# Optimization experiments

Measured on AMD Instinct MI355X. Metric: run time of the kernel, lower is better.

## Reference

```python
import jax, jax.numpy as jnp
import numpy as np

N_NODES = 100000
N_EDGES = 1600000
D_IN, D_HID, D_OUT = 128, 16, 32


def setup_inputs() -> dict:
    key = jax.random.key(0)
    k1, k2, k3, k4, k5 = jax.random.split(key, 5)
    features = jax.random.normal(k1, (N_NODES, D_IN), dtype=jnp.float32)
    src = jax.random.randint(k2, (N_EDGES,), 0, N_NODES, dtype=jnp.int32)
    dst = jax.random.randint(k3, (N_EDGES,), 0, N_NODES, dtype=jnp.int32)
    # linear layer params (PyTorch Linear: y = x @ W.T + b); store as (in, out)
    s1 = 1.0 / np.sqrt(D_IN)
    s2 = 1.0 / np.sqrt(D_HID)
    W1 = jax.random.uniform(k4, (D_IN, D_HID), minval=-s1, maxval=s1, dtype=jnp.float32)
    b1 = jnp.zeros((D_HID,), dtype=jnp.float32)
    W2 = jax.random.uniform(k5, (D_HID, D_OUT), minval=-s2, maxval=s2, dtype=jnp.float32)
    b2 = jnp.zeros((D_OUT,), dtype=jnp.float32)
    return {"features": features, "src": src, "dst": dst,
            "W1": W1, "b1": b1, "W2": W2, "b2": b2}


def _gcn_layer(h, src, dst, W, b):
    # copy_src + sum: aggregate neighbor (src) features onto dst nodes
    agg = jax.ops.segment_sum(h[src], dst, num_segments=N_NODES)
    return agg @ W + b


def reference(features, src, dst, W1, b1, W2, b2):
    x = jax.nn.relu(_gcn_layer(features, src, dst, W1, b1))
    x = _gcn_layer(x, src, dst, W2, b2)
    return x
```

## Files before the change

### kernel.cpp

```cpp
#include <hip/hip_runtime.h>
#include <hip/hip_bf16.h>

#define N_NODES 100000
#define N_EDGES 1600000
#define D_IN    128
#define D_HID   16
#define D_OUT   32

#define BSHIFT 8
#define BNODES 256
#define NB 391
#define NBPAD 512
#define SCHUNK 4096
#define SBLOCKS 391
#define MMBLOCKS 1563
#define SLAB 4608
#define NOSTRIDE 257

#define SS_HIST   0
#define SS_LBASE  2048
#define SS_GBASE  4096
#define SS_TSCAN  5696
#define SS_SORTED 6720
#define SS_BID    23104
#define SS_BYTES  31296

__device__ inline float bf_lo(unsigned dw) { return __uint_as_float(dw << 16); }
__device__ inline float bf_hi(unsigned dw) { return __uint_as_float(dw & 0xffff0000u); }
__device__ inline unsigned bf_pack(float f0, float f1) {
    union { __hip_bfloat16 h[2]; unsigned u; } pu;
    pu.h[0] = __float2bfloat16(f0);
    pu.h[1] = __float2bfloat16(f1);
    return pu.u;
}
__device__ inline void acc4(float* a, uint2 w) {
    a[0] += bf_lo(w.x); a[1] += bf_hi(w.x);
    a[2] += bf_lo(w.y); a[3] += bf_hi(w.y);
}

__global__ __launch_bounds__(256) void k_fused1(const float* __restrict__ feat,
                                                const float* __restrict__ W1,
                                                const int* __restrict__ src,
                                                const int* __restrict__ dst,
                                                int* __restrict__ cursor,
                                                unsigned* __restrict__ pairs,
                                                unsigned* __restrict__ Yu) {
    __shared__ __align__(16) char smem[SS_BYTES];
    int tid = threadIdx.x, blk = blockIdx.x;

    if (blk < SBLOCKS) {
        int* hist    = (int*)(smem + SS_HIST);
        int* lbase   = (int*)(smem + SS_LBASE);
        int* gbase   = (int*)(smem + SS_GBASE);
        int* tscan   = (int*)(smem + SS_TSCAN);
        unsigned* sorted = (unsigned*)(smem + SS_SORTED);
        unsigned short* bId = (unsigned short*)(smem + SS_BID);

        int base = blk * SCHUNK;
        int nval = N_EDGES - base;
        if (nval > SCHUNK) nval = SCHUNK;

        for (int i = tid; i < NBPAD; i += 256) hist[i] = 0;
        __syncthreads();

        int varr[16], barr[16];
#pragma unroll
        for (int k = 0; k < 16; ++k) {
            int e = base + k * 256 + tid;
            if (e < N_EDGES) {
                int s = src[e], d = dst[e];
                varr[k] = (s << BSHIFT) | (d & (BNODES - 1));
                int b = d >> BSHIFT;
                barr[k] = b;
                atomicAdd(&hist[b], 1);
            } else {
                barr[k] = -1;
            }
        }
        __syncthreads();

        int i0 = tid * 2;
        int h0 = hist[i0], h1 = hist[i0 + 1];
        int lsum = h0 + h1;
        tscan[tid] = lsum;
        __syncthreads();
#pragma unroll
        for (int off = 1; off < 256; off <<= 1) {
            int x = (tid >= off) ? tscan[tid - off] : 0;
            __syncthreads();
            tscan[tid] += x;
            __syncthreads();
        }
        int excl = tscan[tid] - lsum;
        lbase[i0 + 0] = excl;
        lbase[i0 + 1] = excl + h0;
        __syncthreads();

        for (int i = tid; i < NB; i += 256) {
            int c = hist[i];
            if (c > 0) gbase[i] = i * SLAB + atomicAdd(&cursor[i], c);
        }
        __syncthreads();
        for (int i = tid; i < NBPAD; i += 256) hist[i] = 0;
        __syncthreads();

#pragma unroll
        for (int k = 0; k < 16; ++k) {
            int b = barr[k];
            if (b >= 0) {
                int r = atomicAdd(&hist[b], 1);
                int p = lbase[b] + r;
                sorted[p] = (unsigned)varr[k];
                bId[p] = (unsigned short)b;
            }
        }
        __syncthreads();

        for (int i = tid; i < nval; i += 256) {
            int b = bId[i];
            pairs[gbase[b] + (i - lbase[b])] = sorted[i];
        }
    } else {
        float* sW = (float*)smem;
        for (int i = tid; i < D_IN * D_HID; i += 256) sW[i] = W1[i];
        __syncthreads();

        int gid = (blk - SBLOCKS) * 256 + tid;
        int n = gid >> 2;
        int jq = gid & 3;
        if (n >= N_NODES) return;

        const float4* f4 = (const float4*)(feat + (size_t)n * D_IN);
        const float4* sW4 = (const float4*)sW;

        float4 acc = make_float4(0.f, 0.f, 0.f, 0.f);
#pragma unroll 8
        for (int kq = 0; kq < 32; ++kq) {
            float4 f = f4[kq];
            int k0 = kq * 4;
            float4 w0 = sW4[(k0 + 0) * 4 + jq];
            float4 w1 = sW4[(k0 + 1) * 4 + jq];
            float4 w2 = sW4[(k0 + 2) * 4 + jq];
            float4 w3 = sW4[(k0 + 3) * 4 + jq];
            acc.x += f.x * w0.x + f.y * w1.x + f.z * w2.x + f.w * w3.x;
            acc.y += f.x * w0.y + f.y * w1.y + f.z * w2.y + f.w * w3.y;
            acc.z += f.x * w0.z + f.y * w1.z + f.z * w2.z + f.w * w3.z;
            acc.w += f.x * w0.w + f.y * w1.w + f.z * w2.w + f.w * w3.w;
        }
        uint2 o;
        o.x = bf_pack(acc.x, acc.y);
        o.y = bf_pack(acc.z, acc.w);
        ((uint2*)(Yu + (size_t)n * 8))[jq] = o;
    }
}

__global__ __launch_bounds__(256) void k_nodesort(const int* __restrict__ cursor,
                                                  unsigned* __restrict__ pairs,
                                                  int* __restrict__ node_off) {
    __shared__ unsigned buf[SLAB];
    __shared__ int hist[BNODES];
    __shared__ int cur[BNODES];
    __shared__ int t[256];

    int tid = threadIdx.x, b = blockIdx.x;
    int beg = b * SLAB;
    int cnt = cursor[b];

    hist[tid] = 0;
    __syncthreads();

    for (int i = tid; i < cnt; i += 256) {
        unsigned p = pairs[beg + i];
        buf[i] = p;
        atomicAdd(&hist[p & (BNODES - 1)], 1);
    }
    __syncthreads();

    int v = hist[tid];
    t[tid] = v;
    __syncthreads();
#pragma unroll
    for (int off = 1; off < 256; off <<= 1) {
        int x = (tid >= off) ? t[tid - off] : 0;
        __syncthreads();
        t[tid] += x;
        __syncthreads();
    }
    int excl = t[tid] - v;
    cur[tid] = excl;
    node_off[b * NOSTRIDE + tid] = beg + excl;
    if (tid == 0) node_off[b * NOSTRIDE + BNODES] = beg + cnt;
    __syncthreads();

    for (int i = tid; i < cnt; i += 256) {
        unsigned p = buf[i];
        int pos = atomicAdd(&cur[p & (BNODES - 1)], 1);
        pairs[beg + pos] = p >> BSHIFT;
    }
}

__global__ __launch_bounds__(256) void k_agg1(const int* __restrict__ node_off,
                                              const unsigned* __restrict__ csr,
                                              const uint2* __restrict__ Yu2,
                                              const float* __restrict__ bias1,
                                              uint2* __restrict__ H1u2) {
    int tid = threadIdx.x;
    int g = tid >> 2, c = tid & 3;
    int n = blockIdx.x * 64 + g;
    if (n >= N_NODES) return;
    int idx = n + (n >> 8);
    int beg = node_off[idx], end = node_off[idx + 1];

    float a[4] = {0.f, 0.f, 0.f, 0.f}, b[4] = {0.f, 0.f, 0.f, 0.f};
    int i = beg;
    for (; i + 7 < end; i += 8) {
        unsigned s0 = csr[i],     s1 = csr[i + 1], s2 = csr[i + 2], s3 = csr[i + 3];
        unsigned s4 = csr[i + 4], s5 = csr[i + 5], s6 = csr[i + 6], s7 = csr[i + 7];
        uint2 w0 = Yu2[(size_t)s0 * 4 + c];
        uint2 w1 = Yu2[(size_t)s1 * 4 + c];
        uint2 w2 = Yu2[(size_t)s2 * 4 + c];
        uint2 w3 = Yu2[(size_t)s3 * 4 + c];
        uint2 w4 = Yu2[(size_t)s4 * 4 + c];
        uint2 w5 = Yu2[(size_t)s5 * 4 + c];
        uint2 w6 = Yu2[(size_t)s6 * 4 + c];
        uint2 w7 = Yu2[(size_t)s7 * 4 + c];
        acc4(a, w0); acc4(b, w1); acc4(a, w2); acc4(b, w3);
        acc4(a, w4); acc4(b, w5); acc4(a, w6); acc4(b, w7);
    }
    for (; i < end; ++i) {
        uint2 w = Yu2[(size_t)csr[i] * 4 + c];
        acc4(a, w);
    }
    float f0 = a[0] + b[0] + bias1[c * 4 + 0];
    float f1 = a[1] + b[1] + bias1[c * 4 + 1];
    float f2 = a[2] + b[2] + bias1[c * 4 + 2];
    float f3 = a[3] + b[3] + bias1[c * 4 + 3];
    uint2 o;
    o.x = bf_pack(fmaxf(f0, 0.f), fmaxf(f1, 0.f));
    o.y = bf_pack(fmaxf(f2, 0.f), fmaxf(f3, 0.f));
    H1u2[(size_t)n * 4 + c] = o;
}

__global__ __launch_bounds__(256) void k_agg2(const int* __restrict__ node_off,
                                              const unsigned* __restrict__ csr,
                                              const uint2* __restrict__ H1u2,
                                              const float* __restrict__ W2,
                                              const float* __restrict__ b2,
                                              float* __restrict__ out) {
    __shared__ float sacc[64][D_HID + 1];
    __shared__ float sW2[D_HID * D_OUT];
    __shared__ float sb2[D_OUT];
    int tid = threadIdx.x;
    for (int i2 = tid; i2 < D_HID * D_OUT; i2 += 256) sW2[i2] = W2[i2];
    if (tid < D_OUT) sb2[tid] = b2[tid];

    int g = tid >> 2, c = tid & 3;
    int n = blockIdx.x * 64 + g;

    float a[4] = {0.f, 0.f, 0.f, 0.f}, b[4] = {0.f, 0.f, 0.f, 0.f};
    if (n < N_NODES) {
        int idx = n + (n >> 8);
        int beg = node_off[idx], end = node_off[idx + 1];
        int i = beg;
        for (; i + 7 < end; i += 8) {
            unsigned s0 = csr[i],     s1 = csr[i + 1], s2 = csr[i + 2], s3 = csr[i + 3];
            unsigned s4 = csr[i + 4], s5 = csr[i + 5], s6 = csr[i + 6], s7 = csr[i + 7];
            uint2 w0 = H1u2[(size_t)s0 * 4 + c];
            uint2 w1 = H1u2[(size_t)s1 * 4 + c];
            uint2 w2 = H1u2[(size_t)s2 * 4 + c];
            uint2 w3 = H1u2[(size_t)s3 * 4 + c];
            uint2 w4 = H1u2[(size_t)s4 * 4 + c];
            uint2 w5 = H1u2[(size_t)s5 * 4 + c];
            uint2 w6 = H1u2[(size_t)s6 * 4 + c];
            uint2 w7 = H1u2[(size_t)s7 * 4 + c];
            acc4(a, w0); acc4(b, w1); acc4(a, w2); acc4(b, w3);
            acc4(a, w4); acc4(b, w5); acc4(a, w6); acc4(b, w7);
        }
        for (; i < end; ++i) {
            uint2 w = H1u2[(size_t)csr[i] * 4 + c];
            acc4(a, w);
        }
    }
    sacc[g][c * 4 + 0] = a[0] + b[0];
    sacc[g][c * 4 + 1] = a[1] + b[1];
    sacc[g][c * 4 + 2] = a[2] + b[2];
    sacc[g][c * 4 + 3] = a[3] + b[3];
    __syncthreads();

    for (int t2 = tid; t2 < 64 * D_OUT; t2 += 256) {
        int gg = t2 >> 5, o = t2 & 31;
        int node = blockIdx.x * 64 + gg;
        if (node < N_NODES) {
            float acc = sb2[o];
#pragma unroll
            for (int j = 0; j < D_HID; ++j)
                acc = fmaf(sacc[gg][j], sW2[j * D_OUT + o], acc);
            out[(size_t)node * D_OUT + o] = acc;
        }
    }
}

extern "C" void kernel_launch(void* const* d_in, const int* in_sizes, int n_in,
                              void* d_out, int out_size, void* d_ws, size_t ws_size,
                              hipStream_t stream) {
    const float* feat = (const float*)d_in[0];
    const int*   src  = (const int*)d_in[1];
    const int*   dst  = (const int*)d_in[2];
    const float* W1   = (const float*)d_in[3];
    const float* b1   = (const float*)d_in[4];
    const float* W2   = (const float*)d_in[5];
    const float* b2   = (const float*)d_in[6];
    float* out = (float*)d_out;

    char* base = (char*)d_ws;
    unsigned* pairs    = (unsigned*)(base);
    unsigned* Yu       = (unsigned*)(base + 7208960);
    unsigned* H1u      = (unsigned*)(base + 10408960);
    int*      cursor   = (int*)(base + 13608960);
    int*      node_off = (int*)(base + 13613056);

    hipMemsetAsync(cursor, 0, NB * sizeof(int), stream);

    k_fused1  <<<SBLOCKS + MMBLOCKS, 256, 0, stream>>>(feat, W1, src, dst,
                                                       cursor, pairs, Yu);
    k_nodesort<<<NB, 256, 0, stream>>>(cursor, pairs, node_off);
    k_agg1    <<<(N_NODES + 63) / 64, 256, 0, stream>>>(node_off, pairs,
                                                        (const uint2*)Yu, b1,
                                                        (uint2*)H1u);
    k_agg2    <<<(N_NODES + 63) / 64, 256, 0, stream>>>(node_off, pairs,
                                                        (const uint2*)H1u, W2, b2, out);
}
```

Baseline: 89.73 us.

## Fuse per-bucket node sort with first-layer aggregation in one 1024-thread kernel

```diff
diff --git a/kernel.cpp b/kernel.cpp
--- a/kernel.cpp
+++ b/kernel.cpp
@@ -154,66 +154,69 @@
     }
 }
 
-__global__ __launch_bounds__(256) void k_nodesort(const int* __restrict__ cursor,
-                                                  unsigned* __restrict__ pairs,
-                                                  int* __restrict__ node_off) {
+__global__ __launch_bounds__(1024) void k_sortagg1(const int* __restrict__ cursor,
+                                                   unsigned* __restrict__ pairs,
+                                                   const uint2* __restrict__ Yu2,
+                                                   const float* __restrict__ bias1,
+                                                   uint2* __restrict__ H1u2,
+                                                   int* __restrict__ node_off) {
     __shared__ unsigned buf[SLAB];
     __shared__ int hist[BNODES];
+    __shared__ int lbase[BNODES];
     __shared__ int cur[BNODES];
-    __shared__ int t[256];
+    __shared__ int t[BNODES];
+    __shared__ float sB[D_HID];
 
     int tid = threadIdx.x, b = blockIdx.x;
     int beg = b * SLAB;
     int cnt = cursor[b];
 
-    hist[tid] = 0;
-    __syncthreads();
-
-    for (int i = tid; i < cnt; i += 256) {
+    if (tid < BNODES) hist[tid] = 0;
+    if (tid < D_HID) sB[tid] = bias1[tid];
+    __syncthreads();
+
+    for (int i = tid; i < cnt; i += 1024) {
         unsigned p = pairs[beg + i];
         buf[i] = p;
         atomicAdd(&hist[p & (BNODES - 1)], 1);
     }
     __syncthreads();
 
-    int v = hist[tid];
-    t[tid] = v;
-    __syncthreads();
-#pragma unroll
-    for (int off = 1; off < 256; off <<= 1) {
-        int x = (tid >= off) ? t[tid - off] : 0;
-        __syncthreads();
-        t[tid] += x;
-        __syncthreads();
-    }
-    int excl = t[tid] - v;
-    cur[tid] = excl;
-    node_off[b * NOSTRIDE + tid] = beg + excl;
-    if (tid == 0) node_off[b * NOSTRIDE + BNODES] = beg + cnt;
-    __syncthreads();
-
-    for (int i = tid; i < cnt; i += 256) {
+    if (tid < BNODES) t[tid] = hist[tid];
+    __syncthreads();
+#pragma unroll
+    for (int off = 1; off < BNODES; off <<= 1) {
+        int x = 0;
+        if (tid < BNODES && tid >= off) x = t[tid - off];
+        __syncthreads();
+        if (tid < BNODES) t[tid] += x;
+        __syncthreads();
+    }
+    if (tid < BNODES) {
+        int excl = t[tid] - hist[tid];
+        lbase[tid] = excl;
+        cur[tid] = excl;
+        node_off[b * NOSTRIDE + tid] = beg + excl;
+        if (tid == 0) node_off[b * NOSTRIDE + BNODES] = beg + cnt;
+    }
+    __syncthreads();
+
+    for (int i = tid; i < cnt; i += 1024) {
         unsigned p = buf[i];
         int pos = atomicAdd(&cur[p & (BNODES - 1)], 1);
         pairs[beg + pos] = p >> BSHIFT;
     }
-}
-
-__global__ __launch_bounds__(256) void k_agg1(const int* __restrict__ node_off,
-                                              const unsigned* __restrict__ csr,
-                                              const uint2* __restrict__ Yu2,
-                                              const float* __restrict__ bias1,
-                                              uint2* __restrict__ H1u2) {
-    int tid = threadIdx.x;
+    __syncthreads();
+
     int g = tid >> 2, c = tid & 3;
-    int n = blockIdx.x * 64 + g;
+    int n = b * BNODES + g;
     if (n >= N_NODES) return;
-    int idx = n + (n >> 8);
-    int beg = node_off[idx], end = node_off[idx + 1];
-
-    float a[4] = {0.f, 0.f, 0.f, 0.f}, b[4] = {0.f, 0.f, 0.f, 0.f};
-    int i = beg;
-    for (; i + 7 < end; i += 8) {
+    int i = beg + lbase[g];
+    int e = beg + cur[g];
+    const unsigned* csr = pairs;
+
+    float a[4] = {0.f, 0.f, 0.f, 0.f}, bb[4] = {0.f, 0.f, 0.f, 0.f};
+    for (; i + 7 < e; i += 8) {
         unsigned s0 = csr[i],     s1 = csr[i + 1], s2 = csr[i + 2], s3 = csr[i + 3];
         unsigned s4 = csr[i + 4], s5 = csr[i + 5], s6 = csr[i + 6], s7 = csr[i + 7];
         uint2 w0 = Yu2[(size_t)s0 * 4 + c];
@@ -224,17 +227,25 @@
         uint2 w5 = Yu2[(size_t)s5 * 4 + c];
         uint2 w6 = Yu2[(size_t)s6 * 4 + c];
         uint2 w7 = Yu2[(size_t)s7 * 4 + c];
-        acc4(a, w0); acc4(b, w1); acc4(a, w2); acc4(b, w3);
-        acc4(a, w4); acc4(b, w5); acc4(a, w6); acc4(b, w7);
-    }
-    for (; i < end; ++i) {
+        acc4(a, w0); acc4(bb, w1); acc4(a, w2); acc4(bb, w3);
+        acc4(a, w4); acc4(bb, w5); acc4(a, w6); acc4(bb, w7);
+    }
+    for (; i + 3 < e; i += 4) {
+        unsigned s0 = csr[i], s1 = csr[i + 1], s2 = csr[i + 2], s3 = csr[i + 3];
+        uint2 w0 = Yu2[(size_t)s0 * 4 + c];
+        uint2 w1 = Yu2[(size_t)s1 * 4 + c];
+        uint2 w2 = Yu2[(size_t)s2 * 4 + c];
+        uint2 w3 = Yu2[(size_t)s3 * 4 + c];
+        acc4(a, w0); acc4(bb, w1); acc4(a, w2); acc4(bb, w3);
+    }
+    for (; i < e; ++i) {
         uint2 w = Yu2[(size_t)csr[i] * 4 + c];
         acc4(a, w);
     }
-    float f0 = a[0] + b[0] + bias1[c * 4 + 0];
-    float f1 = a[1] + b[1] + bias1[c * 4 + 1];
-    float f2 = a[2] + b[2] + bias1[c * 4 + 2];
-    float f3 = a[3] + b[3] + bias1[c * 4 + 3];
+    float f0 = a[0] + bb[0] + sB[c * 4 + 0];
+    float f1 = a[1] + bb[1] + sB[c * 4 + 1];
+    float f2 = a[2] + bb[2] + sB[c * 4 + 2];
+    float f3 = a[3] + bb[3] + sB[c * 4 + 3];
     uint2 o;
     o.x = bf_pack(fmaxf(f0, 0.f), fmaxf(f1, 0.f));
     o.y = bf_pack(fmaxf(f2, 0.f), fmaxf(f3, 0.f));
@@ -257,12 +268,11 @@
     int g = tid >> 2, c = tid & 3;
     int n = blockIdx.x * 64 + g;
 
-    float a[4] = {0.f, 0.f, 0.f, 0.f}, b[4] = {0.f, 0.f, 0.f, 0.f};
+    float a[4] = {0.f, 0.f, 0.f, 0.f}, bb[4] = {0.f, 0.f, 0.f, 0.f};
     if (n < N_NODES) {
         int idx = n + (n >> 8);
-        int beg = node_off[idx], end = node_off[idx + 1];
-        int i = beg;
-        for (; i + 7 < end; i += 8) {
+        int i = node_off[idx], e = node_off[idx + 1];
+        for (; i + 7 < e; i += 8) {
             unsigned s0 = csr[i],     s1 = csr[i + 1], s2 = csr[i + 2], s3 = csr[i + 3];
             unsigned s4 = csr[i + 4], s5 = csr[i + 5], s6 = csr[i + 6], s7 = csr[i + 7];
             uint2 w0 = H1u2[(size_t)s0 * 4 + c];
@@ -273,18 +283,26 @@
             uint2 w5 = H1u2[(size_t)s5 * 4 + c];
             uint2 w6 = H1u2[(size_t)s6 * 4 + c];
             uint2 w7 = H1u2[(size_t)s7 * 4 + c];
-            acc4(a, w0); acc4(b, w1); acc4(a, w2); acc4(b, w3);
-            acc4(a, w4); acc4(b, w5); acc4(a, w6); acc4(b, w7);
-        }
-        for (; i < end; ++i) {
+            acc4(a, w0); acc4(bb, w1); acc4(a, w2); acc4(bb, w3);
+            acc4(a, w4); acc4(bb, w5); acc4(a, w6); acc4(bb, w7);
+        }
+        for (; i + 3 < e; i += 4) {
+            unsigned s0 = csr[i], s1 = csr[i + 1], s2 = csr[i + 2], s3 = csr[i + 3];
+            uint2 w0 = H1u2[(size_t)s0 * 4 + c];
+            uint2 w1 = H1u2[(size_t)s1 * 4 + c];
+            uint2 w2 = H1u2[(size_t)s2 * 4 + c];
+            uint2 w3 = H1u2[(size_t)s3 * 4 + c];
+            acc4(a, w0); acc4(bb, w1); acc4(a, w2); acc4(bb, w3);
+        }
+        for (; i < e; ++i) {
             uint2 w = H1u2[(size_t)csr[i] * 4 + c];
             acc4(a, w);
         }
     }
-    sacc[g][c * 4 + 0] = a[0] + b[0];
-    sacc[g][c * 4 + 1] = a[1] + b[1];
-    sacc[g][c * 4 + 2] = a[2] + b[2];
-    sacc[g][c * 4 + 3] = a[3] + b[3];
+    sacc[g][c * 4 + 0] = a[0] + bb[0];
+    sacc[g][c * 4 + 1] = a[1] + bb[1];
+    sacc[g][c * 4 + 2] = a[2] + bb[2];
+    sacc[g][c * 4 + 3] = a[3] + bb[3];
     __syncthreads();
 
     for (int t2 = tid; t2 < 64 * D_OUT; t2 += 256) {
@@ -321,12 +339,10 @@
 
     hipMemsetAsync(cursor, 0, NB * sizeof(int), stream);
 
-    k_fused1  <<<SBLOCKS + MMBLOCKS, 256, 0, stream>>>(feat, W1, src, dst,
-                                                       cursor, pairs, Yu);
-    k_nodesort<<<NB, 256, 0, stream>>>(cursor, pairs, node_off);
-    k_agg1    <<<(N_NODES + 63) / 64, 256, 0, stream>>>(node_off, pairs,
-                                                        (const uint2*)Yu, b1,
-                                                        (uint2*)H1u);
-    k_agg2    <<<(N_NODES + 63) / 64, 256, 0, stream>>>(node_off, pairs,
-                                                        (const uint2*)H1u, W2, b2, out);
-}
+    k_fused1   <<<SBLOCKS + MMBLOCKS, 256, 0, stream>>>(feat, W1, src, dst,
+                                                        cursor, pairs, Yu);
+    k_sortagg1 <<<NB, 1024, 0, stream>>>(cursor, pairs, (const uint2*)Yu, b1,
+                                         (uint2*)H1u, node_off);
+    k_agg2     <<<(N_NODES + 63) / 64, 256, 0, stream>>>(node_off, pairs,
+                                                         (const uint2*)H1u, W2, b2, out);
+}
```

Result: faster. 83.71 us (-6.7%).
